# Optimization experiments

Hardware: AMD Instinct MI355X
Metric: run time of the kernel (lower is better)

Reference implementation:

```python
import jax, jax.numpy as jnp
import numpy as np

RES = (32, 32, 32)   # S, H, W
WS = 4               # window size (cubic)
SHIFT = 2            # shift size
NH = 6               # num heads
C = 192              # dim
EPS = 1e-5


def _rel_pos_index(ws):
    coords = np.stack(np.meshgrid(np.arange(ws), np.arange(ws), np.arange(ws), indexing='ij'))
    cf = coords.reshape(3, -1)                      # (3, N)
    rc = (cf[:, :, None] - cf[:, None, :]).transpose(1, 2, 0).astype(np.int64)  # (N,N,3)
    rc[..., 0] += ws - 1
    rc[..., 1] += ws - 1
    rc[..., 2] += ws - 1
    rc[..., 0] *= 3 * ws - 1
    rc[..., 1] *= 2 * ws - 1
    return rc.sum(-1)                               # (N, N)

_RPI = jnp.asarray(_rel_pos_index(WS))


def _ln(x, g, b):
    m = jnp.mean(x, axis=-1, keepdims=True)
    v = jnp.mean(jnp.square(x - m), axis=-1, keepdims=True)
    return (x - m) * jax.lax.rsqrt(v + EPS) * g + b


def setup_inputs():
    key = jax.random.key(0)
    ks = jax.random.split(key, 12)
    B, L = 2, RES[0] * RES[1] * RES[2]
    nW, N = 512, WS ** 3
    Hd = 4 * C
    p = lambda k, s: jax.random.normal(k, s, jnp.float32) * 0.02
    return {
        'x': jax.random.normal(ks[0], (B, L, C), jnp.float32),
        'mask_matrix': jax.random.normal(ks[1], (nW, N, N), jnp.float32),
        'skip': jax.random.normal(ks[2], (B, L, C), jnp.float32),
        'x_up': jax.random.normal(ks[3], (B, L, C), jnp.float32),
        'norm1_g': jnp.ones((C,), jnp.float32), 'norm1_b': jnp.zeros((C,), jnp.float32),
        'kv_w': p(ks[4], (C, 2 * C)), 'kv_b': jnp.zeros((2 * C,), jnp.float32),
        'rpb_table': p(ks[5], ((2 * WS - 1) ** 3, NH)),
        'proj_w': p(ks[6], (C, C)), 'proj_b': jnp.zeros((C,), jnp.float32),
        'norm2_g': jnp.ones((C,), jnp.float32), 'norm2_b': jnp.zeros((C,), jnp.float32),
        'fc1_w': p(ks[7], (C, Hd)), 'fc1_b': jnp.zeros((Hd,), jnp.float32),
        'fc2_w': p(ks[8], (Hd, C)), 'fc2_b': jnp.zeros((C,), jnp.float32),
    }


def reference(x, mask_matrix, skip, x_up, norm1_g, norm1_b, kv_w, kv_b, rpb_table,
              proj_w, proj_b, norm2_g, norm2_b, fc1_w, fc1_b, fc2_w, fc2_b):
    B, L, _ = x.shape
    S, H, W = RES
    ws, N = WS, WS ** 3
    hd = C // NH
    scale = hd ** -0.5

    sn = _ln(skip, norm1_g, norm1_b).reshape(B, S, H, W, C)
    qn = _ln(x_up, norm1_g, norm1_b).reshape(B, S, H, W, C)
    # cyclic shift (shift_size > 0)
    sn = jnp.roll(sn, (-SHIFT, -SHIFT, -SHIFT), axis=(1, 2, 3))
    qn = jnp.roll(qn, (-SHIFT, -SHIFT, -SHIFT), axis=(1, 2, 3))

    def part(t):  # window partition -> (B*nW, N, C)
        t = t.reshape(B, S // ws, ws, H // ws, ws, W // ws, ws, C)
        return t.transpose(0, 1, 3, 5, 2, 4, 6, 7).reshape(-1, N, C)

    skw, qw = part(sn), part(qn)
    B_ = skw.shape[0]

    kv = (skw @ kv_w + kv_b).reshape(B_, N, 2, NH, hd)
    k = kv[:, :, 0].transpose(0, 2, 1, 3)   # (B_, NH, N, hd)
    v = kv[:, :, 1].transpose(0, 2, 1, 3)
    q = qw.reshape(B_, N, NH, hd).transpose(0, 2, 1, 3) * scale

    attn = jnp.einsum('bhqd,bhkd->bhqk', q, k)
    rpb = rpb_table[_RPI.reshape(-1)].reshape(N, N, NH).transpose(2, 0, 1)  # (NH, N, N)
    attn = attn + rpb[None]
    nW = mask_matrix.shape[0]
    attn = attn.reshape(B, nW, NH, N, N) + mask_matrix[None, :, None]
    attn = jax.nn.softmax(attn.reshape(B_, NH, N, N), axis=-1)

    out = jnp.einsum('bhqk,bhkd->bhqd', attn, v).transpose(0, 2, 1, 3).reshape(B_, N, C)
    out = out @ proj_w + proj_b

    # window reverse
    out = out.reshape(B, S // ws, H // ws, W // ws, ws, ws, ws, C)
    out = out.transpose(0, 1, 4, 2, 5, 3, 6, 7).reshape(B, S, H, W, C)
    out = jnp.roll(out, (SHIFT, SHIFT, SHIFT), axis=(1, 2, 3)).reshape(B, L, C)

    x = x + out
    h = _ln(x, norm2_g, norm2_b)
    h = jax.nn.gelu(h @ fc1_w + fc1_b, approximate=False) @ fc2_w + fc2_b
    return x + h
```

## Files before the change

### kernel.cpp

```cpp
#include <hip/hip_runtime.h>
#include <math.h>

typedef unsigned short u16;
typedef __bf16 bf16x8 __attribute__((ext_vector_type(8)));
typedef float f32x4 __attribute__((ext_vector_type(4)));
typedef unsigned short u16x8 __attribute__((ext_vector_type(8)));

#define SHIFT 2

static __device__ __forceinline__ f32x4 mfma16(bf16x8 a, bf16x8 b, f32x4 c) {
  return __builtin_amdgcn_mfma_f32_16x16x32_bf16(a, b, c, 0, 0, 0);
}
static __device__ __forceinline__ u16 f2bf(float f) {
  unsigned u = __builtin_bit_cast(unsigned, f);
  unsigned r = u + 0x7fffu + ((u >> 16) & 1u);
  return (u16)(r >> 16);
}
static __device__ __forceinline__ float bf2f(u16 u) {
  unsigned v = (unsigned)u << 16;
  return __builtin_bit_cast(float, v);
}
static __device__ __forceinline__ void stage16(const u16* g, u16* lbase, int lane) {
#if __has_builtin(__builtin_amdgcn_global_load_lds)
  __builtin_amdgcn_global_load_lds(
      (const __attribute__((address_space(1))) unsigned int*)g,
      (__attribute__((address_space(3))) unsigned int*)lbase, 16, 0, 0);
#else
  *(u16x8*)(lbase + lane * 8) = *(const u16x8*)g;
#endif
}

#define OFF_KVWT  ((size_t)0)
#define OFF_PRWT  (OFF_KVWT + 384*192*2)
#define OFF_FC1WT (OFF_PRWT + 192*192*2)
#define OFF_FC2WT (OFF_FC1WT + 768*192*2)
#define OFF_SKW   (OFF_FC2WT + 192*768*2)
#define OFF_QW    (OFF_SKW + (size_t)65536*192*2)
#define OFF_KVB   (OFF_QW + (size_t)65536*192*2)
#define OFF_POX   (OFF_KVB + (size_t)65536*384*2)
#define OFF_YB    (OFF_POX + (size_t)65536*192*2)
#define OFF_HN    (OFF_YB + (size_t)65536*192*2)
#define OFF_RPBG  (OFF_HN + (size_t)65536*192*2)

__global__ __launch_bounds__(256) void k_prep(
    const float* __restrict__ kv_w, const float* __restrict__ proj_w,
    const float* __restrict__ fc1_w, const float* __restrict__ fc2_w,
    const float* __restrict__ rpb,
    u16* __restrict__ kvT, u16* __restrict__ prT,
    u16* __restrict__ f1T, u16* __restrict__ f2T, u16* __restrict__ rpbg) {
  int i = blockIdx.x * 256 + threadIdx.x;
  if (i < 192 * 384) kvT[(i % 384) * 192 + i / 384] = f2bf(kv_w[i]);
  if (i < 192 * 192) prT[(i % 192) * 192 + i / 192] = f2bf(proj_w[i]);
  if (i < 192 * 768) f1T[(i % 768) * 192 + i / 768] = f2bf(fc1_w[i]);
  if (i < 768 * 192) f2T[(i % 192) * 768 + i / 192] = f2bf(fc2_w[i]);
  if (i < 24576) {
    int h = i >> 12, rem = i & 4095, qr = rem >> 6, kc = rem & 63;
    int qs = qr >> 4, qh = (qr >> 2) & 3, qx = qr & 3;
    int ks = kc >> 4, kh = (kc >> 2) & 3, kx = kc & 3;
    int idx = (qs - ks + 3) * 11 + (qh - kh + 3) * 7 + (qx - kx + 3);
    rpbg[i] = f2bf(rpb[idx * 6 + h]);
  }
}

__global__ __launch_bounds__(256) void k_ln_part(
    const float* __restrict__ skip, const float* __restrict__ x_up,
    const float* __restrict__ gam, const float* __restrict__ bet,
    u16* __restrict__ skw, u16* __restrict__ qw) {
  int row = blockIdx.x * 4 + (threadIdx.x >> 6);
  int lane = threadIdx.x & 63;
  const float* sp = skip + (size_t)row * 192;
  const float* qp = x_up + (size_t)row * 192;
  float sv[3], qv[3], ss = 0.f, qs = 0.f;
#pragma unroll
  for (int j = 0; j < 3; j++) {
    sv[j] = sp[lane + 64 * j]; qv[j] = qp[lane + 64 * j];
    ss += sv[j]; qs += qv[j];
  }
#pragma unroll
  for (int m = 1; m < 64; m <<= 1) { ss += __shfl_xor(ss, m, 64); qs += __shfl_xor(qs, m, 64); }
  float sm = ss * (1.f / 192.f), qm = qs * (1.f / 192.f);
  float s2 = 0.f, q2 = 0.f;
#pragma unroll
  for (int j = 0; j < 3; j++) { float d = sv[j] - sm; s2 += d * d; d = qv[j] - qm; q2 += d * d; }
#pragma unroll
  for (int m = 1; m < 64; m <<= 1) { s2 += __shfl_xor(s2, m, 64); q2 += __shfl_xor(q2, m, 64); }
  float sr = rsqrtf(s2 * (1.f / 192.f) + 1e-5f), qr = rsqrtf(q2 * (1.f / 192.f) + 1e-5f);
  int b = row >> 15, l = row & 32767;
  int s = l >> 10, h = (l >> 5) & 31, w = l & 31;
  int s_ = (s - SHIFT) & 31, h_ = (h - SHIFT) & 31, w_ = (w - SHIFT) & 31;
  int wIdx = ((s_ >> 2) * 8 + (h_ >> 2)) * 8 + (w_ >> 2);
  int n = ((s_ & 3) * 4 + (h_ & 3)) * 4 + (w_ & 3);
  size_t orow = ((size_t)(b * 512 + wIdx) * 64 + n) * 192;
  const float scale = 0.17677669529663687f;
#pragma unroll
  for (int j = 0; j < 3; j++) {
    int cc = lane + 64 * j;
    float gg = gam[cc], bb = bet[cc];
    skw[orow + cc] = f2bf((sv[j] - sm) * sr * gg + bb);
    qw[orow + cc]  = f2bf(((qv[j] - qm) * qr * gg + bb) * scale);
  }
}

__global__ __launch_bounds__(256, 2) void k_kv(
    const u16* __restrict__ A, const u16* __restrict__ BT,
    const float* __restrict__ bias, u16* __restrict__ outh) {
  __shared__ u16 lw[192 * 192];
  int mb = blockIdx.x, nb = blockIdx.y;
  int tid = threadIdx.x, l = tid & 63, wv = tid >> 6, g = l >> 4, c = l & 15;
  int wr = wv >> 1, wc = wv & 1;
#pragma unroll
  for (int i = 0; i < 18; i++) {
    int CI = i * 256 + tid;
    int row = CI / 24, ch = CI % 24;
    int sch = (ch & 24) | ((ch ^ row) & 7);
    stage16(BT + (size_t)(nb * 192 + row) * 192 + sch * 8, lw + (i * 256 + wv * 64) * 8, l);
  }
  __syncthreads();
  f32x4 acc[4][6] = {};
#pragma unroll
  for (int ks = 0; ks < 6; ks++) {
    bf16x8 a[4];
#pragma unroll
    for (int m = 0; m < 4; m++)
      a[m] = *(const bf16x8*)&A[(size_t)(mb * 128 + wr * 64 + m * 16 + c) * 192 + ks * 32 + g * 8];
#pragma unroll
    for (int n = 0; n < 6; n++) {
      int col = wc * 96 + n * 16 + c;
      int ch = ks * 4 + g;
      int chp = (ch & 24) | ((ch ^ col) & 7);
      bf16x8 b = *(const bf16x8*)&lw[col * 192 + chp * 8];
#pragma unroll
      for (int m = 0; m < 4; m++) acc[m][n] = mfma16(a[m], b, acc[m][n]);
    }
  }
#pragma unroll
  for (int n = 0; n < 6; n++)
#pragma unroll
    for (int m = 0; m < 4; m++) {
      int col = nb * 192 + wc * 96 + n * 16 + c;
      float bb = bias[col];
#pragma unroll
      for (int r = 0; r < 4; r++) {
        int row = mb * 128 + wr * 64 + m * 16 + g * 4 + r;
        outh[(size_t)row * 384 + col] = f2bf(acc[m][n][r] + bb);
      }
    }
}

__global__ __launch_bounds__(384) void k_attn_mega(
    const u16* __restrict__ qw, const u16* __restrict__ kvb,
    const u16* __restrict__ rpbg, const float* __restrict__ mask,
    const u16* __restrict__ prT, const float* __restrict__ proj_b,
    u16* __restrict__ pox) {
  __shared__ __align__(16) char smem[38400];
  u16* lv = (u16*)smem;
  u16* lo = (u16*)smem;
  u16* lp = (u16*)(smem + 24576);
  int b_ = blockIdx.x, wIdx = b_ & 511;
  int tid = threadIdx.x, l = tid & 63, wv = tid >> 6, g = l >> 4, c = l & 15;
  int h = wv;
#pragma unroll
  for (int i = 0; i < 4; i++) {
    int CI = i * 384 + tid;
    int row = CI / 24, ch = CI % 24;
    stage16(kvb + ((size_t)b_ * 64 + row) * 384 + 192 + ch * 8,
            lv + (i * 384 + wv * 64) * 8, l);
  }
  bf16x8 qa[4], kb[4];
#pragma unroll
  for (int m = 0; m < 4; m++)
    qa[m] = *(const bf16x8*)&qw[((size_t)b_ * 64 + m * 16 + c) * 192 + h * 32 + g * 8];
#pragma unroll
  for (int n = 0; n < 4; n++)
    kb[n] = *(const bf16x8*)&kvb[((size_t)b_ * 64 + n * 16 + c) * 384 + h * 32 + g * 8];
  __syncthreads();
  bf16x8 vb[2][2];
#pragma unroll
  for (int kk = 0; kk < 2; kk++)
#pragma unroll
    for (int nd = 0; nd < 2; nd++) {
      union { u16 u[8]; bf16x8 v; } bb;
#pragma unroll
      for (int j = 0; j < 8; j++)
        bb.u[j] = lv[(kk * 32 + g * 8 + j) * 192 + h * 32 + nd * 16 + c];
      vb[kk][nd] = bb.v;
    }
  __syncthreads();
  f32x4 acc[4][4] = {};
#pragma unroll
  for (int m = 0; m < 4; m++)
#pragma unroll
    for (int n = 0; n < 4; n++) acc[m][n] = mfma16(qa[m], kb[n], acc[m][n]);
  const float* mrow = mask + (size_t)wIdx * 4096;
  const u16* rg = rpbg + h * 4096;
  f32x4 oacc[4][2] = {};
#pragma unroll
  for (int m = 0; m < 4; m++) {
#pragma unroll
    for (int r = 0; r < 4; r++) {
      int qr = m * 16 + g * 4 + r;
      float vals[4];
#pragma unroll
      for (int n = 0; n < 4; n++) {
        int kc = n * 16 + c;
        vals[n] = acc[m][n][r] + bf2f(rg[qr * 64 + kc]) + mrow[qr * 64 + kc];
      }
      float mx = fmaxf(fmaxf(vals[0], vals[1]), fmaxf(vals[2], vals[3]));
#pragma unroll
      for (int mm = 1; mm < 16; mm <<= 1) mx = fmaxf(mx, __shfl_xor(mx, mm, 64));
      float sum = 0.f;
#pragma unroll
      for (int n = 0; n < 4; n++) { vals[n] = __expf(vals[n] - mx); sum += vals[n]; }
#pragma unroll
      for (int mm = 1; mm < 16; mm <<= 1) sum += __shfl_xor(sum, mm, 64);
      float inv = 1.f / sum;
#pragma unroll
      for (int n = 0; n < 4; n++)
        lp[h * 1152 + (g * 4 + r) * 72 + n * 16 + c] = f2bf(vals[n] * inv);
    }
#pragma unroll
    for (int kk = 0; kk < 2; kk++) {
      bf16x8 pa = *(const bf16x8*)&lp[h * 1152 + c * 72 + kk * 32 + g * 8];
#pragma unroll
      for (int nd = 0; nd < 2; nd++) oacc[m][nd] = mfma16(pa, vb[kk][nd], oacc[m][nd]);
    }
  }
  __syncthreads();
#pragma unroll
  for (int m = 0; m < 4; m++)
#pragma unroll
    for (int nd = 0; nd < 2; nd++)
#pragma unroll
      for (int r = 0; r < 4; r++)
        lo[(m * 16 + g * 4 + r) * 200 + h * 32 + nd * 16 + c] = f2bf(oacc[m][nd][r]);
  __syncthreads();
  f32x4 pacc[4][2] = {};
#pragma unroll
  for (int ks = 0; ks < 6; ks++) {
    bf16x8 pa[4];
#pragma unroll
    for (int m = 0; m < 4; m++)
      pa[m] = *(const bf16x8*)&lo[(m * 16 + c) * 200 + ks * 32 + g * 8];
#pragma unroll
    for (int n = 0; n < 2; n++) {
      bf16x8 pb = *(const bf16x8*)&prT[(size_t)(wv * 32 + n * 16 + c) * 192 + ks * 32 + g * 8];
#pragma unroll
      for (int m = 0; m < 4; m++) pacc[m][n] = mfma16(pa[m], pb, pacc[m][n]);
    }
  }
#pragma unroll
  for (int m = 0; m < 4; m++)
#pragma unroll
    for (int r = 0; r < 4; r++) {
      int tok = m * 16 + g * 4 + r;
#pragma unroll
      for (int n = 0; n < 2; n++) {
        int col = wv * 32 + n * 16 + c;
        pox[((size_t)b_ * 64 + tok) * 192 + col] = f2bf(pacc[m][n][r] + proj_b[col]);
      }
    }
}

__global__ __launch_bounds__(256) void k_ln2(
    const float* __restrict__ x, const u16* __restrict__ pox,
    const float* __restrict__ g2, const float* __restrict__ b2,
    u16* __restrict__ yb, u16* __restrict__ hn) {
  int row = blockIdx.x * 4 + (threadIdx.x >> 6);
  int lane = threadIdx.x & 63;
  int b = row >> 15, ll = row & 32767;
  int s = ll >> 10, hh = (ll >> 5) & 31, w = ll & 31;
  int s_ = (s - SHIFT) & 31, h_ = (hh - SHIFT) & 31, w_ = (w - SHIFT) & 31;
  int wI = ((s_ >> 2) * 8 + (h_ >> 2)) * 8 + (w_ >> 2);
  int n = ((s_ & 3) * 4 + (h_ & 3)) * 4 + (w_ & 3);
  size_t wrow = ((size_t)(b * 512 + wI) * 64 + n) * 192;
  float y[3]; float ss = 0.f, sq = 0.f;
#pragma unroll
  for (int j = 0; j < 3; j++) {
    int cc = lane + 64 * j;
    y[j] = x[(size_t)row * 192 + cc] + bf2f(pox[wrow + cc]);
    ss += y[j]; sq += y[j] * y[j];
  }
#pragma unroll
  for (int m = 1; m < 64; m <<= 1) { ss += __shfl_xor(ss, m, 64); sq += __shfl_xor(sq, m, 64); }
  float mu = ss * (1.f / 192.f);
  float rs = rsqrtf(sq * (1.f / 192.f) - mu * mu + 1e-5f);
#pragma unroll
  for (int j = 0; j < 3; j++) {
    int cc = lane + 64 * j;
    yb[(size_t)row * 192 + cc] = f2bf(y[j]);
    hn[(size_t)row * 192 + cc] = f2bf((y[j] - mu) * rs * g2[cc] + b2[cc]);
  }
}

__global__ __launch_bounds__(256) void k_mlp(
    const u16* __restrict__ hn, const u16* __restrict__ f1T,
    const u16* __restrict__ f2T, const float* __restrict__ b1,
    const float* __restrict__ b2f, const u16* __restrict__ yb,
    float* __restrict__ out) {
  __shared__ u16 lds[29184];
  u16* f1c = lds;
  u16* f2c = lds + 12288;
  u16* h1c = lds + 24576;
  int tid = threadIdx.x, l = tid & 63, wv = tid >> 6, g = l >> 4, c = l & 15;
  size_t tokbase = (size_t)blockIdx.x * 64;
#pragma unroll
  for (int i = 0; i < 6; i++) {
    int CI = i * 256 + wv * 64 + l;
    int row = CI / 24, chp = CI % 24;
    int sch = (chp & 24) | ((chp ^ row) & 7);
    stage16(hn + (tokbase + row) * 192 + sch * 8, f1c + (i * 256 + wv * 64) * 8, l);
  }
  __syncthreads();
  bf16x8 hb[4][6];
#pragma unroll
  for (int tf = 0; tf < 4; tf++)
#pragma unroll
    for (int ks = 0; ks < 6; ks++) {
      int ch = ks * 4 + g;
      int chp = (ch & 24) | ((ch ^ c) & 7);
      hb[tf][ks] = *(const bf16x8*)&f1c[(tf * 16 + c) * 192 + chp * 8];
    }
  f32x4 acc2[3][4] = {};
#pragma unroll 1
  for (int ko = 0; ko < 12; ko++) {
    __syncthreads();
#pragma unroll
    for (int i = 0; i < 6; i++) {
      int CI = i * 256 + wv * 64 + l;
      int row = CI / 24, chp = CI % 24;
      int sch = (chp & 24) | ((chp ^ row) & 7);
      stage16(f1T + (size_t)(ko * 64 + row) * 192 + sch * 8,
              f1c + (i * 256 + wv * 64) * 8, l);
    }
#pragma unroll
    for (int i = 0; i < 6; i++) {
      int CI = i * 256 + wv * 64 + l;
      int row = CI >> 3, chp = CI & 7;
      int sch = chp ^ (row & 7);
      stage16(f2T + (size_t)row * 768 + ko * 64 + sch * 8,
              f2c + (i * 256 + wv * 64) * 8, l);
    }
    __syncthreads();
    f32x4 acc1[4] = {};
#pragma unroll
    for (int ks = 0; ks < 6; ks++) {
      int ch = ks * 4 + g;
      int chp = (ch & 24) | ((ch ^ c) & 7);
      bf16x8 wa = *(const bf16x8*)&f1c[(wv * 16 + c) * 192 + chp * 8];
#pragma unroll
      for (int tf = 0; tf < 4; tf++) acc1[tf] = mfma16(wa, hb[tf][ks], acc1[tf]);
    }
    float4 b1v = *(const float4*)&b1[ko * 64 + wv * 16 + g * 4];
#pragma unroll
    for (int tf = 0; tf < 4; tf++) {
      unsigned pk[2];
#pragma unroll
      for (int p = 0; p < 2; p++) {
        unsigned lohi[2];
#pragma unroll
        for (int q = 0; q < 2; q++) {
          int r = p * 2 + q;
          float v = acc1[tf][r] + (r == 0 ? b1v.x : r == 1 ? b1v.y : r == 2 ? b1v.z : b1v.w);
          float u2 = v * (1.5957691216f + 0.0713548163f * v * v);
          v = v * (1.f / (1.f + __expf(-u2)));
          lohi[q] = f2bf(v);
        }
        pk[p] = lohi[0] | (lohi[1] << 16);
      }
      *(uint2*)&h1c[(tf * 16 + c) * 72 + wv * 16 + g * 4] = make_uint2(pk[0], pk[1]);
    }
    __syncthreads();
#pragma unroll
    for (int ck = 0; ck < 2; ck++) {
      bf16x8 a2[4];
#pragma unroll
      for (int tf = 0; tf < 4; tf++)
        a2[tf] = *(const bf16x8*)&h1c[(tf * 16 + c) * 72 + ck * 32 + g * 8];
#pragma unroll
      for (int of = 0; of < 3; of++) {
        int ch = ck * 4 + g;
        int chp = ch ^ (c & 7);
        bf16x8 wb = *(const bf16x8*)&f2c[(wv * 48 + of * 16 + c) * 64 + chp * 8];
#pragma unroll
        for (int tf = 0; tf < 4; tf++) acc2[of][tf] = mfma16(a2[tf], wb, acc2[of][tf]);
      }
    }
  }
#pragma unroll
  for (int of = 0; of < 3; of++)
#pragma unroll
    for (int tf = 0; tf < 4; tf++) {
      int col = wv * 48 + of * 16 + c;
      float bb = b2f[col];
#pragma unroll
      for (int r = 0; r < 4; r++) {
        size_t tok = tokbase + tf * 16 + g * 4 + r;
        size_t base = tok * 192 + col;
        out[base] = acc2[of][tf][r] + bb + bf2f(yb[base]);
      }
    }
}

extern "C" void kernel_launch(void* const* d_in, const int* in_sizes, int n_in,
                              void* d_out, int out_size, void* d_ws, size_t ws_size,
                              hipStream_t stream) {
  const float* x      = (const float*)d_in[0];
  const float* mask   = (const float*)d_in[1];
  const float* skip   = (const float*)d_in[2];
  const float* x_up   = (const float*)d_in[3];
  const float* n1g    = (const float*)d_in[4];
  const float* n1b    = (const float*)d_in[5];
  const float* kv_w   = (const float*)d_in[6];
  const float* kv_b   = (const float*)d_in[7];
  const float* rpb    = (const float*)d_in[8];
  const float* proj_w = (const float*)d_in[9];
  const float* proj_b = (const float*)d_in[10];
  const float* n2g    = (const float*)d_in[11];
  const float* n2b    = (const float*)d_in[12];
  const float* fc1_w  = (const float*)d_in[13];
  const float* fc1_b  = (const float*)d_in[14];
  const float* fc2_w  = (const float*)d_in[15];
  const float* fc2_b  = (const float*)d_in[16];
  char* ws = (char*)d_ws;
  u16* kvT  = (u16*)(ws + OFF_KVWT);
  u16* prT  = (u16*)(ws + OFF_PRWT);
  u16* f1T  = (u16*)(ws + OFF_FC1WT);
  u16* f2T  = (u16*)(ws + OFF_FC2WT);
  u16* skw  = (u16*)(ws + OFF_SKW);
  u16* qw   = (u16*)(ws + OFF_QW);
  u16* kvb  = (u16*)(ws + OFF_KVB);
  u16* pox  = (u16*)(ws + OFF_POX);
  u16* yb   = (u16*)(ws + OFF_YB);
  u16* hn   = (u16*)(ws + OFF_HN);
  u16* rpbg = (u16*)(ws + OFF_RPBG);
  float* out = (float*)d_out;

  k_prep<<<dim3(576), dim3(256), 0, stream>>>(kv_w, proj_w, fc1_w, fc2_w, rpb,
                                              kvT, prT, f1T, f2T, rpbg);
  k_ln_part<<<dim3(16384), dim3(256), 0, stream>>>(skip, x_up, n1g, n1b, skw, qw);
  k_kv<<<dim3(512, 2), dim3(256), 0, stream>>>(skw, kvT, kv_b, kvb);
  k_attn_mega<<<dim3(1024), dim3(384), 0, stream>>>(
      qw, kvb, rpbg, mask, prT, proj_b, pox);
  k_ln2<<<dim3(16384), dim3(256), 0, stream>>>(x, pox, n2g, n2b, yb, hn);
  k_mlp<<<dim3(1024), dim3(256), 0, stream>>>(
      hn, f1T, f2T, fc1_b, fc2_b, yb, out);
}
```

Measured before the change: 269.4 us.

## Transpose QK^T MFMA so softmax rows reduce in-lane with vectorized mask loads

Swaps the MFMA operands so each lane holds four consecutive key columns of one query row. The row max and sum then mostly reduce in registers, needing two cross-lane shuffles instead of four per row. Mask and relative-position bias become vector loads (float4/ushort4), the mask is prefetched early to overlap with the staging, and probabilities go to LDS as packed 64-bit stores. The cost is more registers held live for the prefetched mask (64 floats per thread), which may lower occupancy.

```diff
diff --git a/kernel.cpp b/kernel.cpp
--- a/kernel.cpp
+++ b/kernel.cpp
@@ -166,6 +166,13 @@
     stage16(kvb + ((size_t)b_ * 64 + row) * 384 + 192 + ch * 8,
             lv + (i * 384 + wv * 64) * 8, l);
   }
+  const float* mrow = mask + (size_t)wIdx * 4096;
+  float4 mv[4][4];
+#pragma unroll
+  for (int n = 0; n < 4; n++)
+#pragma unroll
+    for (int m = 0; m < 4; m++)
+      mv[n][m] = *(const float4*)&mrow[(n * 16 + c) * 64 + m * 16 + g * 4];
   bf16x8 qa[4], kb[4];
 #pragma unroll
   for (int m = 0; m < 4; m++)
@@ -190,39 +197,48 @@
 #pragma unroll
   for (int m = 0; m < 4; m++)
 #pragma unroll
-    for (int n = 0; n < 4; n++) acc[m][n] = mfma16(qa[m], kb[n], acc[m][n]);
-  const float* mrow = mask + (size_t)wIdx * 4096;
+    for (int n = 0; n < 4; n++) acc[m][n] = mfma16(kb[m], qa[n], acc[m][n]);
   const u16* rg = rpbg + h * 4096;
   f32x4 oacc[4][2] = {};
 #pragma unroll
-  for (int m = 0; m < 4; m++) {
-#pragma unroll
-    for (int r = 0; r < 4; r++) {
-      int qr = m * 16 + g * 4 + r;
-      float vals[4];
-#pragma unroll
-      for (int n = 0; n < 4; n++) {
-        int kc = n * 16 + c;
-        vals[n] = acc[m][n][r] + bf2f(rg[qr * 64 + kc]) + mrow[qr * 64 + kc];
-      }
-      float mx = fmaxf(fmaxf(vals[0], vals[1]), fmaxf(vals[2], vals[3]));
-#pragma unroll
-      for (int mm = 1; mm < 16; mm <<= 1) mx = fmaxf(mx, __shfl_xor(mx, mm, 64));
-      float sum = 0.f;
-#pragma unroll
-      for (int n = 0; n < 4; n++) { vals[n] = __expf(vals[n] - mx); sum += vals[n]; }
-#pragma unroll
-      for (int mm = 1; mm < 16; mm <<= 1) sum += __shfl_xor(sum, mm, 64);
-      float inv = 1.f / sum;
-#pragma unroll
-      for (int n = 0; n < 4; n++)
-        lp[h * 1152 + (g * 4 + r) * 72 + n * 16 + c] = f2bf(vals[n] * inv);
+  for (int n = 0; n < 4; n++) {
+    ushort4 rv[4];
+#pragma unroll
+    for (int m = 0; m < 4; m++)
+      rv[m] = *(const ushort4*)&rg[(n * 16 + c) * 64 + m * 16 + g * 4];
+    float vals[4][4];
+    float mx = -3.4e38f;
+#pragma unroll
+    for (int m = 0; m < 4; m++) {
+      float mr[4] = {mv[n][m].x, mv[n][m].y, mv[n][m].z, mv[n][m].w};
+      u16 ru[4] = {rv[m].x, rv[m].y, rv[m].z, rv[m].w};
+#pragma unroll
+      for (int r = 0; r < 4; r++) {
+        vals[m][r] = acc[m][n][r] + bf2f(ru[r]) + mr[r];
+        mx = fmaxf(mx, vals[m][r]);
+      }
+    }
+    mx = fmaxf(mx, __shfl_xor(mx, 16, 64));
+    mx = fmaxf(mx, __shfl_xor(mx, 32, 64));
+    float sum = 0.f;
+#pragma unroll
+    for (int m = 0; m < 4; m++)
+#pragma unroll
+      for (int r = 0; r < 4; r++) { vals[m][r] = __expf(vals[m][r] - mx); sum += vals[m][r]; }
+    sum += __shfl_xor(sum, 16, 64);
+    sum += __shfl_xor(sum, 32, 64);
+    float inv = 1.f / sum;
+#pragma unroll
+    for (int m = 0; m < 4; m++) {
+      unsigned p0 = f2bf(vals[m][0] * inv) | ((unsigned)f2bf(vals[m][1] * inv) << 16);
+      unsigned p1 = f2bf(vals[m][2] * inv) | ((unsigned)f2bf(vals[m][3] * inv) << 16);
+      *(uint2*)&lp[h * 1152 + c * 72 + m * 16 + g * 4] = make_uint2(p0, p1);
     }
 #pragma unroll
     for (int kk = 0; kk < 2; kk++) {
       bf16x8 pa = *(const bf16x8*)&lp[h * 1152 + c * 72 + kk * 32 + g * 8];
 #pragma unroll
-      for (int nd = 0; nd < 2; nd++) oacc[m][nd] = mfma16(pa, vb[kk][nd], oacc[m][nd]);
+      for (int nd = 0; nd < 2; nd++) oacc[n][nd] = mfma16(pa, vb[kk][nd], oacc[n][nd]);
     }
   }
   __syncthreads();
```

Measured after the change: 223.3 us. 17.1% less time.
